# Kernel tuning notes

Measured on AMD Instinct MI355X. Metric: run time of the kernel, lower is better.

Reference implementation:

```python
import jax, jax.numpy as jnp
import numpy as np
import math

EMBED = 512
NUM_CLASSES = 100000
BATCH = 512
SCALE = 64.0
MARGIN = 0.5
COS_M = math.cos(MARGIN)
SIN_M = math.sin(MARGIN)
THRESHOLD = math.cos(math.pi - MARGIN)
MARGIN_MULT = math.sin(math.pi - MARGIN) * MARGIN
EPS = 1e-12  # F.normalize eps


def setup_inputs() -> dict:
    key = jax.random.key(0)
    k1, k2, k3 = jax.random.split(key, 3)
    embeddings = jax.random.normal(k1, (BATCH, EMBED), dtype=jnp.float32)
    labels = jax.random.randint(k2, (BATCH,), 0, NUM_CLASSES, dtype=jnp.int64)
    # xavier-uniform-like init for weight (num_classes, embedding_size)
    limit = math.sqrt(6.0 / (NUM_CLASSES + EMBED))
    weight = jax.random.uniform(k3, (NUM_CLASSES, EMBED), dtype=jnp.float32,
                                minval=-limit, maxval=limit)
    return {"embeddings": embeddings, "labels": labels, "weight": weight}


def _l2_normalize(x, axis):
    norm = jnp.sqrt(jnp.sum(x * x, axis=axis, keepdims=True))
    return x / jnp.maximum(norm, EPS)


def reference(embeddings, labels, weight):
    e = _l2_normalize(embeddings, axis=1)          # (B, D)
    w = _l2_normalize(weight, axis=1)              # (C, D)
    cosine = jnp.einsum('bd,cd->bc', e, w)         # (B, C)
    sine = jnp.sqrt(jnp.clip(1.0 - cosine * cosine, 0.0, None))
    phi = cosine * COS_M - sine * SIN_M
    # easy_margin=False branch
    phi = jnp.where(cosine > THRESHOLD, phi, cosine - MARGIN_MULT)
    one_hot = jax.nn.one_hot(labels, NUM_CLASSES, dtype=cosine.dtype)
    logits = SCALE * (one_hot * phi + (1.0 - one_hot) * cosine)
    logp = jax.nn.log_softmax(logits, axis=1)      # (B, C)
    nll = -jnp.take_along_axis(logp, labels[:, None], axis=1)[:, 0]
    return jnp.mean(nll)
```

## Files before the change

### kernel.cpp

```cpp
#include <hip/hip_runtime.h>
#include <hip/hip_bf16.h>
#include <math.h>

#define BATCH 512
#define EMBED 512
#define NCLS  100000
#define NT128 782
#define NBLK  256

typedef __attribute__((ext_vector_type(4)))  float f32x4;
typedef __attribute__((ext_vector_type(16))) float f32x16;
typedef __attribute__((ext_vector_type(2)))  long  i64x2;

constexpr float kCOS_M = 0.8775825618903728f;
constexpr float kSIN_M = 0.4794255386042030f;
constexpr float kTHR   = -0.8775825618903728f;
constexpr float kMM    = 0.2397127693021015f;

#define BARRIER() asm volatile("s_waitcnt lgkmcnt(0)\n\ts_barrier" ::: "memory")

__device__ __forceinline__ unsigned cvt4(float a, float b, float c, float d) {
  int v = __builtin_amdgcn_cvt_pk_fp8_f32(a, b, 0, false);
  v = __builtin_amdgcn_cvt_pk_fp8_f32(c, d, v, true);
  return (unsigned)v;
}

__global__ void knorm_e(const float* __restrict__ E, unsigned char* __restrict__ En8) {
  int r = blockIdx.x;
  int l = threadIdx.x;
  const f32x4* src = (const f32x4*)(E + r * EMBED);
  f32x4 a = src[2 * l], b = src[2 * l + 1];
  float ss = a.x*a.x + a.y*a.y + a.z*a.z + a.w*a.w
           + b.x*b.x + b.y*b.y + b.z*b.z + b.w*b.w;
#pragma unroll
  for (int d = 1; d < 64; d <<= 1) ss += __shfl_xor(ss, d);
  float s = 16.0f / fmaxf(sqrtf(ss), 1e-12f);
  uint2 pk;
  pk.x = cvt4(a.x * s, a.y * s, a.z * s, a.w * s);
  pk.y = cvt4(b.x * s, b.y * s, b.z * s, b.w * s);
  int slotL = (l & 1) * 16 + (l >> 2);
  int half  = (l >> 1) & 1;
  *(uint2*)(En8 + r * 512 + (((slotL ^ (r & 31)) << 4) | (half << 3))) = pk;
}

__global__ void klabel(const float* __restrict__ E, const float* __restrict__ W,
                       const int* __restrict__ labels,
                       float* __restrict__ lcos, float* __restrict__ lphi)
{
  int r = blockIdx.x * 8 + (threadIdx.x >> 6);
  int l = threadIdx.x & 63;
  int lbl = labels[r];
  const float* ep = E + (size_t)r * EMBED + l * 8;
  const float* wp = W + (size_t)lbl * EMBED + l * 8;
  f32x4 e0 = *(const f32x4*)ep, e1 = *(const f32x4*)(ep + 4);
  f32x4 w0 = *(const f32x4*)wp, w1 = *(const f32x4*)(wp + 4);
  float dot = e0.x*w0.x + e0.y*w0.y + e0.z*w0.z + e0.w*w0.w
            + e1.x*w1.x + e1.y*w1.y + e1.z*w1.z + e1.w*w1.w;
  float se = e0.x*e0.x + e0.y*e0.y + e0.z*e0.z + e0.w*e0.w
           + e1.x*e1.x + e1.y*e1.y + e1.z*e1.z + e1.w*e1.w;
  float sw = w0.x*w0.x + w0.y*w0.y + w0.z*w0.z + w0.w*w0.w
           + w1.x*w1.x + w1.y*w1.y + w1.z*w1.z + w1.w*w1.w;
#pragma unroll
  for (int d = 1; d < 64; d <<= 1) {
    dot += __shfl_xor(dot, d); se += __shfl_xor(se, d); sw += __shfl_xor(sw, d);
  }
  float cosv = dot / (fmaxf(sqrtf(se), 1e-12f) * fmaxf(sqrtf(sw), 1e-12f));
  float cc = fminf(fmaxf(cosv, -1.f), 1.f);
  float sine = sqrtf(fmaxf(1.f - cc * cc, 0.f));
  float phi = (cosv > kTHR) ? (cosv * kCOS_M - sine * kSIN_M) : (cosv - kMM);
  if (l == 0) { lcos[r] = 64.f * cosv; lphi[r] = 64.f * phi; }
}

__global__ __launch_bounds__(1024, 4) void kmain(
    const unsigned char* __restrict__ En8, const float* __restrict__ W,
    float* __restrict__ psum, float* __restrict__ rowsumG)
{
  __shared__ __align__(16) unsigned char SH[163840];
  unsigned char* Asm = SH;
  unsigned char* Bb0 = SH + 131072;
  unsigned char* Bb1 = SH + 131072 + 8192;
  unsigned char* Bb2 = SH + 131072 + 16384;
  unsigned char* Bb3 = SH + 131072 + 24576;

  int bid = blockIdx.x;
  int xcd = bid & 7;
  int panel = (bid >> 3) & 1;
  int grp = bid >> 4;
  int cg = xcd | (grp << 3);

  int tid = threadIdx.x;
  int w = tid >> 6, l = tid & 63;
  int wr = w >> 1, wc = w & 1;
  int cl = l & 31, hi = l >> 5;
  int bcls = tid >> 3, bs3 = tid & 7;

  int nt = (cg < 14) ? 7 : 6;
  int nph = nt * 8;
  int R = nt * 4;

#pragma unroll
  for (int i = 0; i < 8; ++i) {
    int base = i * 16384 + w * 1024;
    __builtin_amdgcn_global_load_lds(
        (const __attribute__((address_space(1))) void*)(En8 + panel * 131072 + base + l * 16),
        (__attribute__((address_space(3))) void*)(&Asm[base]), 16, 0, 0);
  }

  float ssq = 0.f;
  const int boffA = (bcls >> 6) * 4096 + ((bs3 & 1) * 2 + (bs3 >> 2)) * 1024
                  + (bcls & 63) * 16 + ((bs3 >> 1) & 1) * 8;

  auto loadB = [&](int q, f32x4& v0, f32x4& v1) {
    int cls = (cg + ((q >> 3) << 7)) * 128 + bcls;
    if (cls >= NCLS) cls = NCLS - 1;
    const float* p = W + (size_t)cls * EMBED + ((q & 7) << 6) + bs3 * 8;
    v0 = *(const f32x4*)p;
    v1 = *(const f32x4*)(p + 4);
  };
  auto writeB = [&](unsigned char* buf, f32x4 v0, f32x4 v1) {
    float x0 = v0.x*128.f, x1 = v0.y*128.f, x2 = v0.z*128.f, x3 = v0.w*128.f;
    float x4 = v1.x*128.f, x5 = v1.y*128.f, x6 = v1.z*128.f, x7 = v1.w*128.f;
    ssq += x0*x0 + x1*x1 + x2*x2 + x3*x3 + x4*x4 + x5*x5 + x6*x6 + x7*x7;
    uint2 pk;
    pk.x = cvt4(x0, x1, x2, x3);
    pk.y = cvt4(x4, x5, x6, x7);
    *(uint2*)(buf + boffA) = pk;
  };

  f32x16 acc0, acc1, S;
#pragma unroll
  for (int e = 0; e < 16; ++e) { acc0[e] = 0.f; acc1[e] = 0.f; S[e] = 0.f; }

  const unsigned char* Abase = Asm + (wr * 32 + cl) * 512;
  const int bcol = wc * 4096 + hi * 2048 + cl * 16;
  const unsigned char* Bc0 = Bb0 + bcol;
  const unsigned char* Bc1 = Bb1 + bcol;
  const unsigned char* Bc2 = Bb2 + bcol;
  const unsigned char* Bc3 = Bb3 + bcol;

  auto compute = [&](const unsigned char* bb, int pt) {
    int t0 = pt * 2;
    i64x2 a0 = *(const i64x2*)(Abase + ((((hi << 4) | t0)       ^ cl) << 4));
    i64x2 a1 = *(const i64x2*)(Abase + ((((hi << 4) | (t0 + 1)) ^ cl) << 4));
    i64x2 b0 = *(const i64x2*)(bb);
    i64x2 b1 = *(const i64x2*)(bb + 1024);
    i64x2 c0 = *(const i64x2*)(bb + 512);
    i64x2 c1 = *(const i64x2*)(bb + 1536);
    __builtin_amdgcn_s_setprio(1);
    acc0 = __builtin_amdgcn_mfma_f32_32x32x16_fp8_fp8(a0[0], b0[0], acc0, 0, 0, 0);
    acc0 = __builtin_amdgcn_mfma_f32_32x32x16_fp8_fp8(a0[1], b0[1], acc0, 0, 0, 0);
    acc0 = __builtin_amdgcn_mfma_f32_32x32x16_fp8_fp8(a1[0], b1[0], acc0, 0, 0, 0);
    acc0 = __builtin_amdgcn_mfma_f32_32x32x16_fp8_fp8(a1[1], b1[1], acc0, 0, 0, 0);
    acc1 = __builtin_amdgcn_mfma_f32_32x32x16_fp8_fp8(a0[0], c0[0], acc1, 0, 0, 0);
    acc1 = __builtin_amdgcn_mfma_f32_32x32x16_fp8_fp8(a0[1], c0[1], acc1, 0, 0, 0);
    acc1 = __builtin_amdgcn_mfma_f32_32x32x16_fp8_fp8(a1[0], c1[0], acc1, 0, 0, 0);
    acc1 = __builtin_amdgcn_mfma_f32_32x32x16_fp8_fp8(a1[1], c1[1], acc1, 0, 0, 0);
    __builtin_amdgcn_s_setprio(0);
  };

  auto ssqred = [&]() {
    float sq = ssq;
    sq += __shfl_xor(sq, 1); sq += __shfl_xor(sq, 2); sq += __shfl_xor(sq, 4);
    if (bs3 == 0) rowsumG[bid * 128 + bcls] = sq;
    ssq = 0.f;
    asm volatile("s_waitcnt vmcnt(0)" ::: "memory");
  };

  float Rrs0 = 1.0f, Rrs1 = 1.0f;
  auto epilogue = [&](int T) {
    float rn0 = 4.0f / sqrtf(fmaxf(Rrs0, 1e-30f));
    float rn1 = 4.0f / sqrtf(fmaxf(Rrs1, 1e-30f));
    int base = (cg + (T << 7)) * 128 + wc * 64;
    float vm0 = (base + cl < NCLS) ? 1.0f : 0.0f;
    float vm1 = (base + 32 + cl < NCLS) ? 1.0f : 0.0f;
#pragma unroll
    for (int e = 0; e < 16; ++e) {
      float u0 = __expf(fmaf(acc0[e], rn0, -64.0f));
      float u1 = __expf(fmaf(acc1[e], rn1, -64.0f));
      S[e] = fmaf(u0, vm0, fmaf(u1, vm1, S[e]));
      acc0[e] = 0.f; acc1[e] = 0.f;
    }
  };

  f32x4 Ae0, Ae1, Ao0, Ao1, Be0, Be1, Bo0, Bo1;

  loadB(0, Ae0, Ae1); loadB(1, Ao0, Ao1);
  writeB(Bb0, Ae0, Ae1); writeB(Bb1, Ao0, Ao1);
  loadB(2, Ae0, Ae1); loadB(3, Ao0, Ao1);
  loadB(4, Be0, Be1); loadB(5, Bo0, Bo1);
  asm volatile("s_waitcnt vmcnt(0)" ::: "memory");
  BARRIER();

  for (int k = 0; k < R; k += 2) {
    {
      int p0 = 2 * k;
      compute(Bc0, p0 & 7);
      compute(Bc1, (p0 + 1) & 7);
      if (k < R - 1) { writeB(Bb2, Ae0, Ae1); writeB(Bb3, Ao0, Ao1); }
      if ((k & 3) == 2) ssqred();
      loadB(p0 + 6, Ae0, Ae1);
      loadB(p0 + 7, Ao0, Ao1);
      BARRIER();
    }
    {
      int p0 = 2 * k + 2;
      bool epi = ((p0 + 1) & 7) == 7;
      if (epi) {
        Rrs0 = rowsumG[bid * 128 + wc * 64 + cl];
        Rrs1 = rowsumG[bid * 128 + wc * 64 + 32 + cl];
      }
      compute(Bc2, p0 & 7);
      compute(Bc3, (p0 + 1) & 7);
      if (epi) epilogue((p0 + 1) >> 3);
      if (k < R - 2) { writeB(Bb0, Be0, Be1); writeB(Bb1, Bo0, Bo1); }
      loadB(p0 + 6, Be0, Be1);
      loadB(p0 + 7, Bo0, Bo1);
      BARRIER();
    }
  }

#pragma unroll
  for (int e = 0; e < 16; ++e) {
    float v = S[e];
    v += __shfl_xor(v, 1); v += __shfl_xor(v, 2); v += __shfl_xor(v, 4);
    v += __shfl_xor(v, 8); v += __shfl_xor(v, 16);
    S[e] = v;
  }
  if (cl == 0) {
#pragma unroll
    for (int e = 0; e < 16; ++e) {
      int row = wr * 32 + (e & 3) + 8 * (e >> 2) + 4 * hi;
      psum[bid * 512 + wc * 256 + row] = S[e];
    }
  }
}

__global__ void kred1(const float* __restrict__ psum, float* __restrict__ pp2) {
  int g = blockIdx.x;
  int r = threadIdx.x;
  int panel = g >> 4, grp = g & 15;
  float s = 0.f;
#pragma unroll
  for (int x = 0; x < 8; ++x) {
    int bid = x | (panel << 3) | (grp << 4);
    s += psum[bid * 512 + r] + psum[bid * 512 + 256 + r];
  }
  pp2[g * 256 + r] = s;
}

__global__ void kfinal(const float* __restrict__ pp2, const float* __restrict__ lcos,
                       const float* __restrict__ lphi, float* __restrict__ out)
{
  int tid = threadIdx.x;
  int panel = tid >> 8, rl = tid & 255;
  float S = 0.f;
#pragma unroll
  for (int grp = 0; grp < 16; ++grp)
    S += pp2[(panel * 16 + grp) * 256 + rl];
  float lc = lcos[tid], lp = lphi[tid];
  S = S - __expf(lc - 64.f) + __expf(lp - 64.f);
  float nll = 64.f + __logf(S) - lp;
#pragma unroll
  for (int d = 1; d < 64; d <<= 1) nll += __shfl_xor(nll, d);
  __shared__ float sm[8];
  if ((tid & 63) == 0) sm[tid >> 6] = nll;
  __syncthreads();
  if (tid == 0) {
    float t = 0.f;
    for (int k = 0; k < 8; ++k) t += sm[k];
    out[0] = t * (1.0f / 512.0f);
  }
}

extern "C" void kernel_launch(void* const* d_in, const int* in_sizes, int n_in,
                              void* d_out, int out_size, void* d_ws, size_t ws_size,
                              hipStream_t stream)
{
  const float* E      = (const float*)d_in[0];
  const int*   labels = (const int*)d_in[1];
  const float* W      = (const float*)d_in[2];
  float* out = (float*)d_out;

  char* ws = (char*)d_ws;
  unsigned char* En8 = (unsigned char*)ws;
  float* psum    = (float*)(ws + 262144);
  float* rowsumG = (float*)(ws + 786432);
  float* pp2     = (float*)(ws + 917504);
  float* lcos    = (float*)(ws + 950272);
  float* lphi    = lcos + BATCH;

  knorm_e<<<BATCH, 64, 0, stream>>>(E, En8);
  klabel <<<64, 512, 0, stream>>>(E, W, labels, lcos, lphi);
  kmain  <<<NBLK, 1024, 0, stream>>>(En8, W, psum, rowsumG);
  kred1  <<<32, 256, 0, stream>>>(psum, pp2);
  kfinal <<<1, 512, 0, stream>>>(pp2, lcos, lphi, out);
}
```

Before: 82.02 us.

## Precompute fp8 weight tiles in separate pass and stream them via direct-to-LDS loads

Adds a conversion kernel that scales W to fp8 in the MFMA-ready swizzled layout and stores per-row partial squared norms. The main GEMM kernel then fetches B tiles with global_load_lds into a 4-buffer ring and reads row norms from global memory, removing in-loop conversion, register staging and the per-block norm reduction. The separate partial-sum reduction kernel is folded into the final kernel. This trades extra global traffic (writing and re-reading the fp8 copy) and a larger workspace for a simpler, more asynchronous main loop.

```diff
diff --git a/kernel.cpp b/kernel.cpp
--- a/kernel.cpp
+++ b/kernel.cpp
@@ -18,6 +18,8 @@
 constexpr float kMM    = 0.2397127693021015f;
 
 #define BARRIER() asm volatile("s_waitcnt lgkmcnt(0)\n\ts_barrier" ::: "memory")
+#define VMW2() asm volatile("s_waitcnt vmcnt(2)" ::: "memory")
+#define VMW0() asm volatile("s_waitcnt vmcnt(0)" ::: "memory")
 
 __device__ __forceinline__ unsigned cvt4(float a, float b, float c, float d) {
   int v = __builtin_amdgcn_cvt_pk_fp8_f32(a, b, 0, false);
@@ -25,7 +27,7 @@
   return (unsigned)v;
 }
 
-__global__ void knorm_e(const float* __restrict__ E, unsigned char* __restrict__ En8) {
+__global__ void knorm_e(const float* __restrict__ E, unsigned char* __restrict__ E8) {
   int r = blockIdx.x;
   int l = threadIdx.x;
   const f32x4* src = (const f32x4*)(E + r * EMBED);
@@ -40,7 +42,7 @@
   pk.y = cvt4(b.x * s, b.y * s, b.z * s, b.w * s);
   int slotL = (l & 1) * 16 + (l >> 2);
   int half  = (l >> 1) & 1;
-  *(uint2*)(En8 + r * 512 + (((slotL ^ (r & 31)) << 4) | (half << 3))) = pk;
+  *(uint2*)(E8 + r * 512 + (((slotL ^ (r & 31)) << 4) | (half << 3))) = pk;
 }
 
 __global__ void klabel(const float* __restrict__ E, const float* __restrict__ W,
@@ -71,9 +73,36 @@
   if (l == 0) { lcos[r] = 64.f * cosv; lphi[r] = 64.f * phi; }
 }
 
+__global__ __launch_bounds__(1024) void kconv(
+    const float* __restrict__ W, unsigned char* __restrict__ W8,
+    float* __restrict__ rowsumP)
+{
+  int blk = blockIdx.x;
+  int tile = blk >> 3, kq = blk & 7;
+  int tid = threadIdx.x;
+  int cls = tid >> 3, bs3 = tid & 7;
+  int clsg = tile * 128 + cls;
+  bool valid = clsg < NCLS;
+  const float* p = W + (size_t)(valid ? clsg : (NCLS - 1)) * EMBED + kq * 64 + bs3 * 8;
+  f32x4 v0 = *(const f32x4*)p;
+  f32x4 v1 = *(const f32x4*)(p + 4);
+  float x0 = v0.x*128.f, x1 = v0.y*128.f, x2 = v0.z*128.f, x3 = v0.w*128.f;
+  float x4 = v1.x*128.f, x5 = v1.y*128.f, x6 = v1.z*128.f, x7 = v1.w*128.f;
+  if (!valid) { x0=x1=x2=x3=x4=x5=x6=x7=0.f; }
+  float ssq = x0*x0 + x1*x1 + x2*x2 + x3*x3 + x4*x4 + x5*x5 + x6*x6 + x7*x7;
+  uint2 pk;
+  pk.x = cvt4(x0, x1, x2, x3);
+  pk.y = cvt4(x4, x5, x6, x7);
+  int boffA = (cls >> 6) * 4096 + ((bs3 & 1) * 2 + (bs3 >> 2)) * 1024
+            + (cls & 63) * 16 + ((bs3 >> 1) & 1) * 8;
+  *(uint2*)(W8 + (size_t)tile * 65536 + kq * 8192 + boffA) = pk;
+  ssq += __shfl_xor(ssq, 1); ssq += __shfl_xor(ssq, 2); ssq += __shfl_xor(ssq, 4);
+  if (bs3 == 0 && valid) rowsumP[(size_t)clsg * 8 + kq] = ssq;
+}
+
 __global__ __launch_bounds__(1024, 4) void kmain(
-    const unsigned char* __restrict__ En8, const float* __restrict__ W,
-    float* __restrict__ psum, float* __restrict__ rowsumG)
+    const unsigned char* __restrict__ E8, const unsigned char* __restrict__ W8,
+    const float* __restrict__ rowsumP, float* __restrict__ psum)
 {
   __shared__ __align__(16) unsigned char SH[163840];
   unsigned char* Asm = SH;
@@ -92,39 +121,26 @@
   int w = tid >> 6, l = tid & 63;
   int wr = w >> 1, wc = w & 1;
   int cl = l & 31, hi = l >> 5;
-  int bcls = tid >> 3, bs3 = tid & 7;
 
   int nt = (cg < 14) ? 7 : 6;
   int nph = nt * 8;
-  int R = nt * 4;
 
 #pragma unroll
   for (int i = 0; i < 8; ++i) {
     int base = i * 16384 + w * 1024;
     __builtin_amdgcn_global_load_lds(
-        (const __attribute__((address_space(1))) void*)(En8 + panel * 131072 + base + l * 16),
+        (const __attribute__((address_space(1))) void*)(E8 + panel * 131072 + base + l * 16),
         (__attribute__((address_space(3))) void*)(&Asm[base]), 16, 0, 0);
   }
 
-  float ssq = 0.f;
-  const int boffA = (bcls >> 6) * 4096 + ((bs3 & 1) * 2 + (bs3 >> 2)) * 1024
-                  + (bcls & 63) * 16 + ((bs3 >> 1) & 1) * 8;
-
-  auto loadB = [&](int q, f32x4& v0, f32x4& v1) {
-    int cls = (cg + ((q >> 3) << 7)) * 128 + bcls;
-    if (cls >= NCLS) cls = NCLS - 1;
-    const float* p = W + (size_t)cls * EMBED + ((q & 7) << 6) + bs3 * 8;
-    v0 = *(const f32x4*)p;
-    v1 = *(const f32x4*)(p + 4);
-  };
-  auto writeB = [&](unsigned char* buf, f32x4 v0, f32x4 v1) {
-    float x0 = v0.x*128.f, x1 = v0.y*128.f, x2 = v0.z*128.f, x3 = v0.w*128.f;
-    float x4 = v1.x*128.f, x5 = v1.y*128.f, x6 = v1.z*128.f, x7 = v1.w*128.f;
-    ssq += x0*x0 + x1*x1 + x2*x2 + x3*x3 + x4*x4 + x5*x5 + x6*x6 + x7*x7;
-    uint2 pk;
-    pk.x = cvt4(x0, x1, x2, x3);
-    pk.y = cvt4(x4, x5, x6, x7);
-    *(uint2*)(buf + boffA) = pk;
+  auto gldsB = [&](unsigned char* buf, int q) {
+    if (tid < 512) {
+      const unsigned char* src = W8 + (size_t)(cg + ((q >> 3) << 7)) * 65536
+                               + (q & 7) * 8192 + tid * 16;
+      __builtin_amdgcn_global_load_lds(
+          (const __attribute__((address_space(1))) void*)src,
+          (__attribute__((address_space(3))) void*)(buf + tid * 16), 16, 0, 0);
+    }
   };
 
   f32x16 acc0, acc1, S;
@@ -158,18 +174,19 @@
     __builtin_amdgcn_s_setprio(0);
   };
 
-  auto ssqred = [&]() {
-    float sq = ssq;
-    sq += __shfl_xor(sq, 1); sq += __shfl_xor(sq, 2); sq += __shfl_xor(sq, 4);
-    if (bs3 == 0) rowsumG[bid * 128 + bcls] = sq;
-    ssq = 0.f;
-    asm volatile("s_waitcnt vmcnt(0)" ::: "memory");
-  };
-
-  float Rrs0 = 1.0f, Rrs1 = 1.0f;
+  f32x4 Rr0a, Rr0b, Rr1a, Rr1b;
+  auto loadRS = [&](int T) {
+    int base = (cg + (T << 7)) * 128 + wc * 64;
+    const float* rp0 = rowsumP + (size_t)(base + cl) * 8;
+    const float* rp1 = rowsumP + (size_t)(base + 32 + cl) * 8;
+    Rr0a = *(const f32x4*)rp0; Rr0b = *(const f32x4*)(rp0 + 4);
+    Rr1a = *(const f32x4*)rp1; Rr1b = *(const f32x4*)(rp1 + 4);
+  };
   auto epilogue = [&](int T) {
-    float rn0 = 4.0f / sqrtf(fmaxf(Rrs0, 1e-30f));
-    float rn1 = 4.0f / sqrtf(fmaxf(Rrs1, 1e-30f));
+    float rs0 = Rr0a.x + Rr0a.y + Rr0a.z + Rr0a.w + Rr0b.x + Rr0b.y + Rr0b.z + Rr0b.w;
+    float rs1 = Rr1a.x + Rr1a.y + Rr1a.z + Rr1a.w + Rr1b.x + Rr1b.y + Rr1b.z + Rr1b.w;
+    float rn0 = 4.0f / sqrtf(fmaxf(rs0, 1e-30f));
+    float rn1 = 4.0f / sqrtf(fmaxf(rs1, 1e-30f));
     int base = (cg + (T << 7)) * 128 + wc * 64;
     float vm0 = (base + cl < NCLS) ? 1.0f : 0.0f;
     float vm1 = (base + 32 + cl < NCLS) ? 1.0f : 0.0f;
@@ -182,42 +199,27 @@
     }
   };
 
-  f32x4 Ae0, Ae1, Ao0, Ao1, Be0, Be1, Bo0, Bo1;
-
-  loadB(0, Ae0, Ae1); loadB(1, Ao0, Ao1);
-  writeB(Bb0, Ae0, Ae1); writeB(Bb1, Ao0, Ao1);
-  loadB(2, Ae0, Ae1); loadB(3, Ao0, Ao1);
-  loadB(4, Be0, Be1); loadB(5, Bo0, Bo1);
-  asm volatile("s_waitcnt vmcnt(0)" ::: "memory");
+  gldsB(Bb0, 0); gldsB(Bb1, 1); gldsB(Bb2, 2);
+  VMW0();
   BARRIER();
 
-  for (int k = 0; k < R; k += 2) {
-    {
-      int p0 = 2 * k;
-      compute(Bc0, p0 & 7);
-      compute(Bc1, (p0 + 1) & 7);
-      if (k < R - 1) { writeB(Bb2, Ae0, Ae1); writeB(Bb3, Ao0, Ao1); }
-      if ((k & 3) == 2) ssqred();
-      loadB(p0 + 6, Ae0, Ae1);
-      loadB(p0 + 7, Ao0, Ao1);
-      BARRIER();
-    }
-    {
-      int p0 = 2 * k + 2;
-      bool epi = ((p0 + 1) & 7) == 7;
-      if (epi) {
-        Rrs0 = rowsumG[bid * 128 + wc * 64 + cl];
-        Rrs1 = rowsumG[bid * 128 + wc * 64 + 32 + cl];
-      }
-      compute(Bc2, p0 & 7);
-      compute(Bc3, (p0 + 1) & 7);
-      if (epi) epilogue((p0 + 1) >> 3);
-      if (k < R - 2) { writeB(Bb0, Be0, Be1); writeB(Bb1, Bo0, Bo1); }
-      loadB(p0 + 6, Be0, Be1);
-      loadB(p0 + 7, Bo0, Bo1);
-      BARRIER();
-    }
-  }
+#define PH(p, BCOL, BGLDS) {                                   \
+    compute(BCOL, (p) & 7);                                    \
+    if (((p) & 7) == 6) loadRS((p) >> 3);                      \
+    bool more = ((p) + 3 < nph);                               \
+    if (more) gldsB(BGLDS, (p) + 3);                           \
+    if (((p) & 7) == 7) epilogue((p) >> 3);                    \
+    if (more) { VMW2(); } else { VMW0(); }                     \
+    BARRIER();                                                 \
+  }
+
+  for (int pb = 0; pb < nph; pb += 4) {
+    PH(pb + 0, Bc0, Bb3)
+    PH(pb + 1, Bc1, Bb0)
+    PH(pb + 2, Bc2, Bb1)
+    PH(pb + 3, Bc3, Bb2)
+  }
+#undef PH
 
 #pragma unroll
   for (int e = 0; e < 16; ++e) {
@@ -235,28 +237,20 @@
   }
 }
 
-__global__ void kred1(const float* __restrict__ psum, float* __restrict__ pp2) {
-  int g = blockIdx.x;
-  int r = threadIdx.x;
-  int panel = g >> 4, grp = g & 15;
-  float s = 0.f;
-#pragma unroll
-  for (int x = 0; x < 8; ++x) {
-    int bid = x | (panel << 3) | (grp << 4);
-    s += psum[bid * 512 + r] + psum[bid * 512 + 256 + r];
-  }
-  pp2[g * 256 + r] = s;
-}
-
-__global__ void kfinal(const float* __restrict__ pp2, const float* __restrict__ lcos,
+__global__ void kfinal(const float* __restrict__ psum, const float* __restrict__ lcos,
                        const float* __restrict__ lphi, float* __restrict__ out)
 {
   int tid = threadIdx.x;
   int panel = tid >> 8, rl = tid & 255;
   float S = 0.f;
 #pragma unroll
-  for (int grp = 0; grp < 16; ++grp)
-    S += pp2[(panel * 16 + grp) * 256 + rl];
+  for (int grp = 0; grp < 16; ++grp) {
+#pragma unroll
+    for (int x = 0; x < 8; ++x) {
+      int b = x | (panel << 3) | (grp << 4);
+      S += psum[b * 512 + rl] + psum[b * 512 + 256 + rl];
+    }
+  }
   float lc = lcos[tid], lp = lphi[tid];
   S = S - __expf(lc - 64.f) + __expf(lp - 64.f);
   float nll = 64.f + __logf(S) - lp;
@@ -282,16 +276,16 @@
   float* out = (float*)d_out;
 
   char* ws = (char*)d_ws;
-  unsigned char* En8 = (unsigned char*)ws;
-  float* psum    = (float*)(ws + 262144);
-  float* rowsumG = (float*)(ws + 786432);
-  float* pp2     = (float*)(ws + 917504);
-  float* lcos    = (float*)(ws + 950272);
+  unsigned char* E8 = (unsigned char*)ws;
+  unsigned char* W8 = (unsigned char*)(ws + 262144);
+  float* rowsumP = (float*)(ws + 262144 + 51249152);
+  float* psum    = (float*)(ws + 262144 + 51249152 + 3203072);
+  float* lcos    = (float*)(ws + 262144 + 51249152 + 3203072 + 524288);
   float* lphi    = lcos + BATCH;
 
-  knorm_e<<<BATCH, 64, 0, stream>>>(E, En8);
+  knorm_e<<<BATCH, 64, 0, stream>>>(E, E8);
   klabel <<<64, 512, 0, stream>>>(E, W, labels, lcos, lphi);
-  kmain  <<<NBLK, 1024, 0, stream>>>(En8, W, psum, rowsumG);
-  kred1  <<<32, 256, 0, stream>>>(psum, pp2);
-  kfinal <<<1, 512, 0, stream>>>(pp2, lcos, lphi, out);
-}
+  kconv  <<<NT128 * 8, 1024, 0, stream>>>(W, W8, rowsumP);
+  kmain  <<<NBLK, 1024, 0, stream>>>(E8, W8, rowsumP, psum);
+  kfinal <<<1, 512, 0, stream>>>(psum, lcos, lphi, out);
+}
```

Result: slower. 117.6 us (+43.3%).
